# Performance work log

Hardware: AMD Instinct MI355X
Metric: run time of the kernel (lower is better)

The kernel has to match this reference:

```python
import jax, jax.numpy as jnp
import numpy as np

N_ATOMS = 200000
N_BONDS = 300000
E = 600000
D = 128
H = 128
EPS = 1e-5  # BatchNorm1d default eps


def setup_inputs() -> dict:
    key = jax.random.key(0)
    ks = jax.random.split(key, 8)
    x_atoms = jax.random.normal(ks[0], (N_ATOMS, D), jnp.float32)
    x_bonds = jax.random.normal(ks[1], (N_BONDS, D), jnp.float32)
    # atoms -> bonds edges: row0 src atom idx, row1 dst bond idx
    ei_ab = jnp.stack([
        jax.random.randint(ks[2], (E,), 0, N_ATOMS),
        jax.random.randint(ks[3], (E,), 0, N_BONDS),
    ]).astype(jnp.int64)
    # bonds -> atoms edges
    ei_ba = jnp.stack([
        jax.random.randint(ks[4], (E,), 0, N_BONDS),
        jax.random.randint(ks[5], (E,), 0, N_ATOMS),
    ]).astype(jnp.int64)
    xav = float(np.sqrt(6.0 / (D + H)))
    W = jax.random.uniform(ks[6], (H, D), jnp.float32, -xav, xav)   # shared lin_rel
    b = jnp.zeros((H,), jnp.float32)
    Wr = jax.random.uniform(ks[7], (H, D), jnp.float32, -xav, xav)  # res_connection
    br = jnp.zeros((H,), jnp.float32)
    return {
        "x_atoms": x_atoms, "x_bonds": x_bonds,
        "ei_ab": ei_ab, "ei_ba": ei_ba,
        "W": W, "b": b, "Wr": Wr, "br": br,
        "gamma_atoms": jnp.ones((H,), jnp.float32),
        "beta_atoms": jnp.zeros((H,), jnp.float32),
        "gamma_bonds": jnp.ones((H,), jnp.float32),
        "beta_bonds": jnp.zeros((H,), jnp.float32),
    }


def _bn(v, g, bt):
    # BatchNorm1d training-mode math: batch mean, biased variance
    m = v.mean(axis=0)
    var = v.var(axis=0)
    return (v - m) * jax.lax.rsqrt(var + EPS) * g + bt


def reference(x_atoms, x_bonds, ei_ab, ei_ba, W, b, Wr, br,
              gamma_atoms, beta_atoms, gamma_bonds, beta_bonds):
    # shared lin_rel applied to both node types
    h_atoms = x_atoms @ W.T + b   # [N_ATOMS, H]
    h_bonds = x_bonds @ W.T + b   # [N_BONDS, H]

    # message = lin(x_src)[src], aggregate = scatter-add at dst (source_to_target)
    agg_bonds = jax.ops.segment_sum(h_atoms[ei_ab[0]], ei_ab[1], num_segments=N_BONDS)
    agg_atoms = jax.ops.segment_sum(h_bonds[ei_ba[0]], ei_ba[1], num_segments=N_ATOMS)

    # residual: activation(res_connection(x))
    out_atoms = agg_atoms + jax.nn.relu(x_atoms @ Wr.T + br)
    out_bonds = agg_bonds + jax.nn.relu(x_bonds @ Wr.T + br)

    # dropout is identity in eval/deterministic reference
    out_atoms = _bn(out_atoms, gamma_atoms, beta_atoms)
    out_bonds = _bn(out_bonds, gamma_bonds, beta_bonds)
    return out_atoms, out_bonds
```

## Files before the change

kernel.cpp:

```cpp
#include <hip/hip_runtime.h>
#include <stdint.h>

#define NATOMS 200000
#define NBONDS 300000
#define NEDGE  600000
#define NSEG   (NATOMS + NBONDS)
#define DF     128
#define EPS    1e-5f
#define SCHUNK 2048
#define NSBLK  ((NSEG + SCHUNK - 1) / SCHUNK)
#define NBUCK  32
#define NCHA   (NATOMS / 64)
#define NCHB   ((NBONDS + 63) / 64)
#define NCH    (NCHA + NCHB)

typedef __attribute__((ext_vector_type(8))) short bf16x8;
typedef __attribute__((ext_vector_type(4))) float f32x4;
typedef unsigned short u16;

__device__ __forceinline__ short f2b(float f) {
  union { float f; uint32_t u; } v; v.f = f;
  uint32_t r = v.u + 0x7fffu + ((v.u >> 16) & 1u);
  return (short)(r >> 16);
}
__device__ __forceinline__ float bf2f(u16 h) {
  union { uint32_t u; float f; } v; v.u = ((uint32_t)h) << 16; return v.f;
}
__device__ __forceinline__ bf16x8 pack8(float4 u, float4 v) {
  bf16x8 t;
  t[0] = f2b(u.x); t[1] = f2b(u.y); t[2] = f2b(u.z); t[3] = f2b(u.w);
  t[4] = f2b(v.x); t[5] = f2b(v.y); t[6] = f2b(v.z); t[7] = f2b(v.w);
  return t;
}

__global__ void k_prep(const float* __restrict__ W, const float* __restrict__ Wr,
                       u16* __restrict__ Wb, u16* __restrict__ Wrb) {
  int i = blockIdx.x * blockDim.x + threadIdx.x;
  if (i < DF * DF) {
    Wb[i]  = (u16)f2b(W[i]);
    Wrb[i] = (u16)f2b(Wr[i]);
  }
}

__global__ void k_setup(const float* __restrict__ xa, const float* __restrict__ xb,
                        u16* __restrict__ xaT, u16* __restrict__ xbT,
                        const int* __restrict__ ab, const int* __restrict__ ba,
                        int* __restrict__ cnt,
                        const float* __restrict__ W, const float* __restrict__ Wr,
                        u16* __restrict__ Wb, u16* __restrict__ Wrb) {
  const int NA8 = NATOMS * DF / 8;
  const int NT8 = NSEG * DF / 8;
  int bid = blockIdx.x;
  if (bid < 4096) {
    int stride = 4096 * 256;
    for (int i = bid * 256 + threadIdx.x; i < NT8; i += stride) {
      const float* src; u16* dst; int j;
      if (i < NA8) { src = xa; dst = xaT; j = i; }
      else { src = xb; dst = xbT; j = i - NA8; }
      const float4 a = *(const float4*)(src + (size_t)j * 8);
      const float4 b = *(const float4*)(src + (size_t)j * 8 + 4);
      *(bf16x8*)(dst + (size_t)j * 8) = pack8(a, b);
    }
  } else if (bid < 4608) {
    int stride = 512 * 256;
    for (int e = (bid - 4096) * 256 + threadIdx.x; e < 2 * NEDGE; e += stride) {
      int g;
      if (e < NEDGE) g = NATOMS + ab[NEDGE + e];
      else           g = ba[NEDGE + (e - NEDGE)];
      atomicAdd(cnt + g, 1);
    }
  } else {
    int i = (bid - 4608) * 256 + threadIdx.x;
    if (i < DF * DF) {
      Wb[i]  = (u16)f2b(W[i]);
      Wrb[i] = (u16)f2b(Wr[i]);
    }
  }
}

__global__ void k_hist(const int* __restrict__ ab, const int* __restrict__ ba,
                       int* __restrict__ cnt) {
  int stride = gridDim.x * blockDim.x;
  for (int e = blockIdx.x * blockDim.x + threadIdx.x; e < 2 * NEDGE; e += stride) {
    int g;
    if (e < NEDGE) g = NATOMS + ab[NEDGE + e];
    else           g = ba[NEDGE + (e - NEDGE)];
    atomicAdd(cnt + g, 1);
  }
}

__global__ void k_scanA(const int* __restrict__ cnt, int* __restrict__ bsum) {
  __shared__ int wsm[4];
  int t = threadIdx.x;
  int base = blockIdx.x * SCHUNK + t * 8;
  int s = 0;
#pragma unroll
  for (int j = 0; j < 8; ++j) { int i = base + j; if (i < NSEG) s += cnt[i]; }
  for (int d = 1; d < 64; d <<= 1) s += __shfl_xor(s, d);
  if ((t & 63) == 0) wsm[t >> 6] = s;
  __syncthreads();
  if (t == 0) bsum[blockIdx.x] = wsm[0] + wsm[1] + wsm[2] + wsm[3];
}

__global__ void k_scanB(const int* __restrict__ bsum, int* __restrict__ bbase) {
  __shared__ int wsm[4];
  int t = threadIdx.x;
  int lane = t & 63;
  int v = (t < NSBLK) ? bsum[t] : 0;
  int s = v;
  for (int d = 1; d < 64; d <<= 1) { int n = __shfl_up(s, d); if (lane >= d) s += n; }
  if (lane == 63) wsm[t >> 6] = s;
  __syncthreads();
  int wbase = 0;
  for (int w = 0; w < (t >> 6); ++w) wbase += wsm[w];
  if (t < NSBLK) bbase[t] = wbase + s - v;
}

__global__ void k_scanC(const int* __restrict__ cnt, const int* __restrict__ bbase,
                        int* __restrict__ off, int* __restrict__ cursor) {
  __shared__ int wsm[4];
  int t = threadIdx.x;
  int lane = t & 63, wv = t >> 6;
  int base = blockIdx.x * SCHUNK + t * 8;
  int v[8]; int ts = 0;
#pragma unroll
  for (int j = 0; j < 8; ++j) { int i = base + j; v[j] = (i < NSEG) ? cnt[i] : 0; ts += v[j]; }
  int s = ts;
  for (int d = 1; d < 64; d <<= 1) { int n = __shfl_up(s, d); if (lane >= d) s += n; }
  if (lane == 63) wsm[wv] = s;
  __syncthreads();
  int wbase = bbase[blockIdx.x];
  for (int w = 0; w < wv; ++w) wbase += wsm[w];
  int run = wbase + s - ts;
#pragma unroll
  for (int j = 0; j < 8; ++j) {
    int i = base + j;
    if (i < NSEG) { off[i] = run; cursor[i] = run; }
    run += v[j];
  }
}

__global__ void k_fill(const int* __restrict__ ab, const int* __restrict__ ba,
                       int* __restrict__ cursor, int* __restrict__ sorted) {
  int stride = gridDim.x * blockDim.x;
  for (int e = blockIdx.x * blockDim.x + threadIdx.x; e < 2 * NEDGE; e += stride) {
    int g, src;
    if (e < NEDGE) { g = NATOMS + ab[NEDGE + e]; src = ab[e]; }
    else { int e2 = e - NEDGE; g = ba[NEDGE + e2]; src = ba[e2]; }
    int pos = atomicAdd(cursor + g, 1);
    sorted[pos] = src;
  }
}

__global__ __launch_bounds__(256) void k_fuse(
    const u16* __restrict__ xaT, const u16* __restrict__ xbT,
    const int* __restrict__ sorted, const int* __restrict__ off,
    const int* __restrict__ cnt, u16* __restrict__ gT,
    const u16* __restrict__ Wb, const u16* __restrict__ Wrb,
    const float* __restrict__ bb, const float* __restrict__ brb,
    float* __restrict__ stats) {
  __shared__ u16 aggL[64 * DF];

  int tid = threadIdx.x;
  int lane = tid & 63;
  int wv = tid >> 6;
  int r16 = lane & 15, kq = lane >> 4;
  int t016 = wv * 32;
  int qw = tid >> 4;
  int l16 = tid & 15;

  bf16x8 wf[2][4], wrf[2][4];
#pragma unroll
  for (int ti = 0; ti < 2; ++ti) {
#pragma unroll
    for (int kk = 0; kk < 4; ++kk) {
      size_t o = (size_t)(t016 + ti * 16 + r16) * DF + kk * 32 + kq * 8;
      wf[ti][kk]  = *(const bf16x8*)(Wb + o);
      wrf[ti][kk] = *(const bf16x8*)(Wrb + o);
    }
  }
  float bvv0 = bb[t016 + r16],      brr0 = brb[t016 + r16];
  float bvv1 = bb[t016 + 16 + r16], brr1 = brb[t016 + 16 + r16];

  float sA0 = 0.f, sA1 = 0.f, qA0 = 0.f, qA1 = 0.f;
  float sB0 = 0.f, sB1 = 0.f, qB0 = 0.f, qB1 = 0.f;

  for (int c = blockIdx.x; c < NCH; c += gridDim.x) {
    int typ, nrows, goff, base;
    if (c < NCHA) { typ = 0; nrows = NATOMS; goff = 0; base = c * 64; }
    else { typ = 1; nrows = NBONDS; goff = NATOMS; base = (c - NCHA) * 64; }
    const u16* gsrc = typ ? xaT : xbT;
    const u16* xsrc = typ ? xbT : xaT;

    __syncthreads();

#pragma unroll
    for (int i = 0; i < 4; ++i) {
      int r = qw + i * 16;
      int row = base + r;
      if (row < nrows) {
        int gidx = goff + row;
        int start = off[gidx], deg = cnt[gidx];
        float a0 = 0.f, a1 = 0.f, a2 = 0.f, a3 = 0.f;
        float a4 = 0.f, a5 = 0.f, a6 = 0.f, a7 = 0.f;
        int k = 0;
        for (; k + 1 < deg; k += 2) {
          int s0 = sorted[start + k], s1 = sorted[start + k + 1];
          bf16x8 v0 = *(const bf16x8*)(gsrc + (size_t)s0 * DF + l16 * 8);
          bf16x8 v1 = *(const bf16x8*)(gsrc + (size_t)s1 * DF + l16 * 8);
          a0 += bf2f((u16)v0[0]) + bf2f((u16)v1[0]);
          a1 += bf2f((u16)v0[1]) + bf2f((u16)v1[1]);
          a2 += bf2f((u16)v0[2]) + bf2f((u16)v1[2]);
          a3 += bf2f((u16)v0[3]) + bf2f((u16)v1[3]);
          a4 += bf2f((u16)v0[4]) + bf2f((u16)v1[4]);
          a5 += bf2f((u16)v0[5]) + bf2f((u16)v1[5]);
          a6 += bf2f((u16)v0[6]) + bf2f((u16)v1[6]);
          a7 += bf2f((u16)v0[7]) + bf2f((u16)v1[7]);
        }
        if (k < deg) {
          int s0 = sorted[start + k];
          bf16x8 v0 = *(const bf16x8*)(gsrc + (size_t)s0 * DF + l16 * 8);
          a0 += bf2f((u16)v0[0]); a1 += bf2f((u16)v0[1]);
          a2 += bf2f((u16)v0[2]); a3 += bf2f((u16)v0[3]);
          a4 += bf2f((u16)v0[4]); a5 += bf2f((u16)v0[5]);
          a6 += bf2f((u16)v0[6]); a7 += bf2f((u16)v0[7]);
        }
        bf16x8 rr;
        rr[0] = f2b(a0); rr[1] = f2b(a1); rr[2] = f2b(a2); rr[3] = f2b(a3);
        rr[4] = f2b(a4); rr[5] = f2b(a5); rr[6] = f2b(a6); rr[7] = f2b(a7);
        *(bf16x8*)(aggL + r * DF + ((l16 ^ (r & 7)) * 8)) = rr;
      }
    }
    __syncthreads();

#pragma unroll
    for (int rg = 0; rg < 4; ++rg) {
      int rowbase = base + rg * 16;
      if (rowbase < nrows) {
        int lrow = rg * 16 + r16;
        bf16x8 fA[4], fX[4];
#pragma unroll
        for (int kk = 0; kk < 4; ++kk) {
          int c8 = (4 * kk + kq) ^ (r16 & 7);
          fA[kk] = *(const bf16x8*)(aggL + lrow * DF + c8 * 8);
        }
        const u16* xp = xsrc + (size_t)(rowbase + r16) * DF + kq * 8;
#pragma unroll
        for (int kk = 0; kk < 4; ++kk) fX[kk] = *(const bf16x8*)(xp + kk * 32);

        f32x4 w0 = {0.f,0.f,0.f,0.f}, w1 = {0.f,0.f,0.f,0.f};
        f32x4 r0 = {0.f,0.f,0.f,0.f}, r1 = {0.f,0.f,0.f,0.f};
#pragma unroll
        for (int kk = 0; kk < 4; ++kk) {
          w0 = __builtin_amdgcn_mfma_f32_16x16x32_bf16(fA[kk], wf[0][kk], w0, 0, 0, 0);
          w1 = __builtin_amdgcn_mfma_f32_16x16x32_bf16(fA[kk], wf[1][kk], w1, 0, 0, 0);
          r0 = __builtin_amdgcn_mfma_f32_16x16x32_bf16(fX[kk], wrf[0][kk], r0, 0, 0, 0);
          r1 = __builtin_amdgcn_mfma_f32_16x16x32_bf16(fX[kk], wrf[1][kk], r1, 0, 0, 0);
        }

        float cf0 = (float)cnt[goff + rowbase + kq * 4 + 0];
        float cf1 = (float)cnt[goff + rowbase + kq * 4 + 1];
        float cf2 = (float)cnt[goff + rowbase + kq * 4 + 2];
        float cf3 = (float)cnt[goff + rowbase + kq * 4 + 3];

        u16* gp = gT + ((size_t)(goff + rowbase + kq * 4) << 7) + t016 + r16;
        float g0, g1, g2, g3, ss, qq;
        g0 = w0[0] + cf0 * bvv0 + fmaxf(r0[0] + brr0, 0.f);
        g1 = w0[1] + cf1 * bvv0 + fmaxf(r0[1] + brr0, 0.f);
        g2 = w0[2] + cf2 * bvv0 + fmaxf(r0[2] + brr0, 0.f);
        g3 = w0[3] + cf3 * bvv0 + fmaxf(r0[3] + brr0, 0.f);
        gp[0]   = (u16)f2b(g0); gp[128] = (u16)f2b(g1);
        gp[256] = (u16)f2b(g2); gp[384] = (u16)f2b(g3);
        ss = g0 + g1 + g2 + g3;
        qq = g0*g0 + g1*g1 + g2*g2 + g3*g3;
        if (typ) { sB0 += ss; qB0 += qq; } else { sA0 += ss; qA0 += qq; }
        g0 = w1[0] + cf0 * bvv1 + fmaxf(r1[0] + brr1, 0.f);
        g1 = w1[1] + cf1 * bvv1 + fmaxf(r1[1] + brr1, 0.f);
        g2 = w1[2] + cf2 * bvv1 + fmaxf(r1[2] + brr1, 0.f);
        g3 = w1[3] + cf3 * bvv1 + fmaxf(r1[3] + brr1, 0.f);
        gp[16]  = (u16)f2b(g0); gp[144] = (u16)f2b(g1);
        gp[272] = (u16)f2b(g2); gp[400] = (u16)f2b(g3);
        ss = g0 + g1 + g2 + g3;
        qq = g0*g0 + g1*g1 + g2*g2 + g3*g3;
        if (typ) { sB1 += ss; qB1 += qq; } else { sA1 += ss; qA1 += qq; }
      }
    }
  }

  int bkt = blockIdx.x & (NBUCK - 1);
  float* p = stats + (size_t)bkt * 4 * DF;
  {
    float s0 = sA0, q0 = qA0, s1 = sB0, q1 = qB0;
    s0 += __shfl_xor(s0, 16); q0 += __shfl_xor(q0, 16);
    s1 += __shfl_xor(s1, 16); q1 += __shfl_xor(q1, 16);
    s0 += __shfl_xor(s0, 32); q0 += __shfl_xor(q0, 32);
    s1 += __shfl_xor(s1, 32); q1 += __shfl_xor(q1, 32);
    if (kq == 0) {
      int feat = t016 + r16;
      atomicAdd(p + 0 * DF + feat, s0);
      atomicAdd(p + 1 * DF + feat, q0);
      atomicAdd(p + 2 * DF + feat, s1);
      atomicAdd(p + 3 * DF + feat, q1);
    }
  }
  {
    float s0 = sA1, q0 = qA1, s1 = sB1, q1 = qB1;
    s0 += __shfl_xor(s0, 16); q0 += __shfl_xor(q0, 16);
    s1 += __shfl_xor(s1, 16); q1 += __shfl_xor(q1, 16);
    s0 += __shfl_xor(s0, 32); q0 += __shfl_xor(q0, 32);
    s1 += __shfl_xor(s1, 32); q1 += __shfl_xor(q1, 32);
    if (kq == 0) {
      int feat = t016 + 16 + r16;
      atomicAdd(p + 0 * DF + feat, s0);
      atomicAdd(p + 1 * DF + feat, q0);
      atomicAdd(p + 2 * DF + feat, s1);
      atomicAdd(p + 3 * DF + feat, q1);
    }
  }
}

__global__ void k_gather_f(const float* __restrict__ xa, const float* __restrict__ xb,
                           const int* __restrict__ sorted, const int* __restrict__ off,
                           const int* __restrict__ cnt, float* __restrict__ outf) {
  int l32 = threadIdx.x & 31;
  int hwid = (blockIdx.x * blockDim.x + threadIdx.x) >> 5;
  int nhw = (gridDim.x * blockDim.x) >> 5;
  for (int g = hwid; g < NSEG; g += nhw) {
    int start = off[g], deg = cnt[g];
    const float* src = (g < NATOMS) ? xb : xa;
    float a0 = 0.f, a1 = 0.f, a2 = 0.f, a3 = 0.f;
    int k = 0;
    for (; k + 1 < deg; k += 2) {
      int s0 = sorted[start + k], s1 = sorted[start + k + 1];
      float4 v0 = *(const float4*)(src + (size_t)s0 * DF + l32 * 4);
      float4 v1 = *(const float4*)(src + (size_t)s1 * DF + l32 * 4);
      a0 += v0.x + v1.x; a1 += v0.y + v1.y; a2 += v0.z + v1.z; a3 += v0.w + v1.w;
    }
    if (k < deg) {
      int s0 = sorted[start + k];
      float4 v0 = *(const float4*)(src + (size_t)s0 * DF + l32 * 4);
      a0 += v0.x; a1 += v0.y; a2 += v0.z; a3 += v0.w;
    }
    float4 r; r.x = a0; r.y = a1; r.z = a2; r.w = a3;
    *(float4*)(outf + (size_t)g * DF + l32 * 4) = r;
  }
}

__global__ __launch_bounds__(256) void k_gemm0(
    const float* __restrict__ xa, const float* __restrict__ xb,
    float* __restrict__ outf, const int* __restrict__ cnt,
    const u16* __restrict__ Wb, const u16* __restrict__ Wrb,
    const float* __restrict__ bb, const float* __restrict__ brb,
    float* __restrict__ stats) {
  int lane = threadIdx.x & 63;
  int wv = threadIdx.x >> 6;
  int r16 = lane & 15, kq = lane >> 4;
  int t016 = wv * 32;

  bf16x8 wf[2][4], wrf[2][4];
#pragma unroll
  for (int ti = 0; ti < 2; ++ti) {
#pragma unroll
    for (int kk = 0; kk < 4; ++kk) {
      size_t o = (size_t)(t016 + ti * 16 + r16) * DF + kk * 32 + kq * 8;
      wf[ti][kk]  = *(const bf16x8*)(Wb + o);
      wrf[ti][kk] = *(const bf16x8*)(Wrb + o);
    }
  }
  float bvv[2] = { bb[t016 + r16], bb[t016 + 16 + r16] };
  float brr[2] = { brb[t016 + r16], brb[t016 + 16 + r16] };

  float sA[2] = {0.f, 0.f}, qA[2] = {0.f, 0.f};
  float sB[2] = {0.f, 0.f}, qB[2] = {0.f, 0.f};

  for (int c = blockIdx.x; c < NCH; c += gridDim.x) {
    int typ, nrows, goff, base;
    if (c < NCHA) { typ = 0; nrows = NATOMS; goff = 0; base = c * 64; }
    else { typ = 1; nrows = NBONDS; goff = NATOMS; base = (c - NCHA) * 64; }
    const float* xsrc = typ ? xb : xa;

#pragma unroll
    for (int rg = 0; rg < 4; ++rg) {
      int rowbase = base + rg * 16;
      if (rowbase < nrows) {
        int row = rowbase + r16;
        const float* ap = outf + (size_t)(goff + row) * DF + kq * 8;
        const float* xp = xsrc + (size_t)row * DF + kq * 8;
        bf16x8 fA[4], fX[4];
#pragma unroll
        for (int kk = 0; kk < 4; ++kk) {
          fA[kk] = pack8(*(const float4*)(ap + kk * 32), *(const float4*)(ap + kk * 32 + 4));
          fX[kk] = pack8(*(const float4*)(xp + kk * 32), *(const float4*)(xp + kk * 32 + 4));
        }
        __syncthreads();

        f32x4 accW[2], accR[2];
#pragma unroll
        for (int ti = 0; ti < 2; ++ti) {
#pragma unroll
          for (int r = 0; r < 4; ++r) { accW[ti][r] = 0.f; accR[ti][r] = 0.f; }
        }
#pragma unroll
        for (int kk = 0; kk < 4; ++kk) {
#pragma unroll
          for (int ti = 0; ti < 2; ++ti) {
            accW[ti] = __builtin_amdgcn_mfma_f32_16x16x32_bf16(fA[kk], wf[ti][kk], accW[ti], 0, 0, 0);
            accR[ti] = __builtin_amdgcn_mfma_f32_16x16x32_bf16(fX[kk], wrf[ti][kk], accR[ti], 0, 0, 0);
          }
        }
        float cf[4];
#pragma unroll
        for (int r = 0; r < 4; ++r)
          cf[r] = (float)cnt[goff + rowbase + kq * 4 + r];
#pragma unroll
        for (int ti = 0; ti < 2; ++ti) {
          int feat = t016 + ti * 16 + r16;
          float s = 0.f, q = 0.f;
#pragma unroll
          for (int r = 0; r < 4; ++r) {
            int grow = rowbase + kq * 4 + r;
            float gg = accW[ti][r] + cf[r] * bvv[ti] + fmaxf(accR[ti][r] + brr[ti], 0.f);
            outf[(size_t)(goff + grow) * DF + feat] = gg;
            s += gg; q += gg * gg;
          }
          if (typ == 0) { sA[ti] += s; qA[ti] += q; }
          else          { sB[ti] += s; qB[ti] += q; }
        }
      }
    }
  }

  int bkt = blockIdx.x & (NBUCK - 1);
  float* p = stats + (size_t)bkt * 4 * DF;
#pragma unroll
  for (int ti = 0; ti < 2; ++ti) {
    float s0 = sA[ti], q0 = qA[ti], s1 = sB[ti], q1 = qB[ti];
    s0 += __shfl_xor(s0, 16); q0 += __shfl_xor(q0, 16);
    s1 += __shfl_xor(s1, 16); q1 += __shfl_xor(q1, 16);
    s0 += __shfl_xor(s0, 32); q0 += __shfl_xor(q0, 32);
    s1 += __shfl_xor(s1, 32); q1 += __shfl_xor(q1, 32);
    if (kq == 0) {
      int feat = t016 + ti * 16 + r16;
      atomicAdd(p + 0 * DF + feat, s0);
      atomicAdd(p + 1 * DF + feat, q0);
      atomicAdd(p + 2 * DF + feat, s1);
      atomicAdd(p + 3 * DF + feat, q1);
    }
  }
}

__global__ void k_stats(const float* __restrict__ stats,
                        const float* __restrict__ ga, const float* __restrict__ bea,
                        const float* __restrict__ gb, const float* __restrict__ beb,
                        float* __restrict__ scale, float* __restrict__ shift) {
  int tid = threadIdx.x;
  if (tid < 2 * DF) {
    int t = tid >> 7, f = tid & (DF - 1);
    float S = 0.f, SS = 0.f;
    for (int bk = 0; bk < NBUCK; ++bk) {
      const float* p = stats + (size_t)bk * 4 * DF;
      S  += p[(2 * t) * DF + f];
      SS += p[(2 * t + 1) * DF + f];
    }
    float n = t ? (float)NBONDS : (float)NATOMS;
    float mean = S / n;
    float var = SS / n - mean * mean;
    float rstd = rsqrtf(var + EPS);
    float g = t ? gb[f] : ga[f];
    float be = t ? beb[f] : bea[f];
    scale[tid] = rstd * g;
    shift[tid] = be - mean * rstd * g;
  }
}

template<int TIER>
__global__ void k_norm(float* __restrict__ out, const u16* __restrict__ gT,
                       const float* __restrict__ scale, const float* __restrict__ shift) {
  if constexpr (TIER) {
    const size_t nv = (size_t)NSEG * DF / 8;
    size_t stride = (size_t)gridDim.x * blockDim.x;
    for (size_t i = (size_t)blockIdx.x * blockDim.x + threadIdx.x; i < nv; i += stride) {
      size_t e = i * 8;
      int t = e >= (size_t)NATOMS * DF;
      int f = (int)(e & (DF - 1));
      bf16x8 v = *(const bf16x8*)(gT + e);
      const float* sc = scale + t * DF + f;
      const float* sh = shift + t * DF + f;
      float4 o0, o1;
      o0.x = fmaf(bf2f((u16)v[0]), sc[0], sh[0]);
      o0.y = fmaf(bf2f((u16)v[1]), sc[1], sh[1]);
      o0.z = fmaf(bf2f((u16)v[2]), sc[2], sh[2]);
      o0.w = fmaf(bf2f((u16)v[3]), sc[3], sh[3]);
      o1.x = fmaf(bf2f((u16)v[4]), sc[4], sh[4]);
      o1.y = fmaf(bf2f((u16)v[5]), sc[5], sh[5]);
      o1.z = fmaf(bf2f((u16)v[6]), sc[6], sh[6]);
      o1.w = fmaf(bf2f((u16)v[7]), sc[7], sh[7]);
      *(float4*)(out + e) = o0;
      *(float4*)(out + e + 4) = o1;
    }
  } else {
    const size_t nv = (size_t)NSEG * DF / 4;
    size_t stride = (size_t)gridDim.x * blockDim.x;
    for (size_t i = (size_t)blockIdx.x * blockDim.x + threadIdx.x; i < nv; i += stride) {
      size_t e = i * 4;
      int t = e >= (size_t)NATOMS * DF;
      int f = (int)(e & (DF - 1));
      const float* sc = scale + t * DF + f;
      const float* sh = shift + t * DF + f;
      float4 v = ((float4*)out)[i];
      v.x = fmaf(v.x, sc[0], sh[0]);
      v.y = fmaf(v.y, sc[1], sh[1]);
      v.z = fmaf(v.z, sc[2], sh[2]);
      v.w = fmaf(v.w, sc[3], sh[3]);
      ((float4*)out)[i] = v;
    }
  }
}

extern "C" void kernel_launch(void* const* d_in, const int* in_sizes, int n_in,
                              void* d_out, int out_size, void* d_ws, size_t ws_size,
                              hipStream_t stream) {
  const float* xa  = (const float*)d_in[0];
  const float* xb  = (const float*)d_in[1];
  const int*   ab  = (const int*)d_in[2];
  const int*   ba  = (const int*)d_in[3];
  const float* W   = (const float*)d_in[4];
  const float* b   = (const float*)d_in[5];
  const float* Wr  = (const float*)d_in[6];
  const float* br  = (const float*)d_in[7];
  const float* ga  = (const float*)d_in[8];
  const float* bea = (const float*)d_in[9];
  const float* gb  = (const float*)d_in[10];
  const float* beb = (const float*)d_in[11];
  float* out = (float*)d_out;

  char* ws = (char*)d_ws;
  int*   cnt    = (int*)ws;
  int*   off    = (int*)(ws +  2000000);
  int*   cursor = (int*)(ws +  4000000);
  int*   sorted = (int*)(ws +  6000000);
  float* stats  = (float*)(ws + 10800000);
  int*   bsum   = (int*)(ws + 10865536);
  int*   bbase  = (int*)(ws + 10866560);
  u16*   Wbf    = (u16*)(ws + 10867584);
  u16*   Wrbf   = (u16*)(ws + 10900352);
  float* scale  = (float*)(ws + 10933120);
  float* shift  = (float*)(ws + 10934144);
  u16*   gT   = (u16*)(ws + 10935168);
  u16*   xaT  = (u16*)(ws + 138935168);
  u16*   xbT  = (u16*)(ws + 190135168);
  const bool xt = ws_size >= 266935168ull;

  hipMemsetAsync(cnt, 0, 2000000, stream);
  hipMemsetAsync(stats, 0, 65536, stream);

  if (xt) {
    k_setup<<<4672, 256, 0, stream>>>(xa, xb, xaT, xbT, ab, ba, cnt, W, Wr, Wbf, Wrbf);
  } else {
    k_prep<<<64, 256, 0, stream>>>(W, Wr, Wbf, Wrbf);
    k_hist<<<2048, 256, 0, stream>>>(ab, ba, cnt);
  }
  k_scanA<<<NSBLK, 256, 0, stream>>>(cnt, bsum);
  k_scanB<<<1, 256, 0, stream>>>(bsum, bbase);
  k_scanC<<<NSBLK, 256, 0, stream>>>(cnt, bbase, off, cursor);
  k_fill<<<2048, 256, 0, stream>>>(ab, ba, cursor, sorted);

  if (xt) {
    k_fuse<<<2048, 256, 0, stream>>>(xaT, xbT, sorted, off, cnt, gT,
                                     Wbf, Wrbf, b, br, stats);
    k_stats<<<1, 256, 0, stream>>>(stats, ga, bea, gb, beb, scale, shift);
    k_norm<1><<<4096, 256, 0, stream>>>(out, gT, scale, shift);
  } else {
    k_gather_f<<<8192, 256, 0, stream>>>(xa, xb, sorted, off, cnt, out);
    k_gemm0<<<2048, 256, 0, stream>>>(xa, xb, out, cnt, Wbf, Wrbf, b, br, stats);
    k_stats<<<1, 256, 0, stream>>>(stats, ga, bea, gb, beb, scale, shift);
    k_norm<0><<<8192, 256, 0, stream>>>(out, gT, scale, shift);
  }
}
```

Before: 552.6 us.

## Double-buffer aggregation tile and overlap gather with previous chunk's MFMA

Gives the fused kernel two LDS aggregation buffers so the gather of chunk c runs before the MFMA/epilogue of chunk c-1, with one barrier per iteration instead of two. The gather loop is also restructured so each thread walks its four rows together, issuing up to four independent row loads per step to expose more memory-level parallelism. The cost is doubled LDS use (32 KB), more registers for the four accumulators, and predicated work bounded by the largest degree among the four rows.

```diff
diff --git a/kernel.cpp b/kernel.cpp
--- a/kernel.cpp
+++ b/kernel.cpp
@@ -152,6 +152,68 @@
   }
 }
 
+#define PHASE_B(TY, NR, GO, BA, XS, BUF) {                                          \
+  _Pragma("unroll")                                                                 \
+  for (int rg = 0; rg < 4; ++rg) {                                                  \
+    int rowbase = (BA) + rg * 16;                                                   \
+    if (rowbase < (NR)) {                                                           \
+      int lrow = rg * 16 + r16;                                                     \
+      int sx = r16 & 7;                                                             \
+      bf16x8 fA0 = *(const bf16x8*)((BUF) + lrow * DF + (((0  + kq) ^ sx) * 8));    \
+      bf16x8 fA1 = *(const bf16x8*)((BUF) + lrow * DF + (((4  + kq) ^ sx) * 8));    \
+      bf16x8 fA2 = *(const bf16x8*)((BUF) + lrow * DF + (((8  + kq) ^ sx) * 8));    \
+      bf16x8 fA3 = *(const bf16x8*)((BUF) + lrow * DF + (((12 + kq) ^ sx) * 8));    \
+      const u16* xp_ = (XS) + (size_t)(rowbase + r16) * DF + kq * 8;                \
+      bf16x8 fX0 = *(const bf16x8*)(xp_);                                           \
+      bf16x8 fX1 = *(const bf16x8*)(xp_ + 32);                                      \
+      bf16x8 fX2 = *(const bf16x8*)(xp_ + 64);                                      \
+      bf16x8 fX3 = *(const bf16x8*)(xp_ + 96);                                      \
+      f32x4 bw0 = {0.f,0.f,0.f,0.f}, bw1 = {0.f,0.f,0.f,0.f};                       \
+      f32x4 bre0 = {0.f,0.f,0.f,0.f}, bre1 = {0.f,0.f,0.f,0.f};                     \
+      bw0 = __builtin_amdgcn_mfma_f32_16x16x32_bf16(fA0, wf[0][0], bw0, 0,0,0);     \
+      bw1 = __builtin_amdgcn_mfma_f32_16x16x32_bf16(fA0, wf[1][0], bw1, 0,0,0);     \
+      bre0 = __builtin_amdgcn_mfma_f32_16x16x32_bf16(fX0, wrf[0][0], bre0, 0,0,0);  \
+      bre1 = __builtin_amdgcn_mfma_f32_16x16x32_bf16(fX0, wrf[1][0], bre1, 0,0,0);  \
+      bw0 = __builtin_amdgcn_mfma_f32_16x16x32_bf16(fA1, wf[0][1], bw0, 0,0,0);     \
+      bw1 = __builtin_amdgcn_mfma_f32_16x16x32_bf16(fA1, wf[1][1], bw1, 0,0,0);     \
+      bre0 = __builtin_amdgcn_mfma_f32_16x16x32_bf16(fX1, wrf[0][1], bre0, 0,0,0);  \
+      bre1 = __builtin_amdgcn_mfma_f32_16x16x32_bf16(fX1, wrf[1][1], bre1, 0,0,0);  \
+      bw0 = __builtin_amdgcn_mfma_f32_16x16x32_bf16(fA2, wf[0][2], bw0, 0,0,0);     \
+      bw1 = __builtin_amdgcn_mfma_f32_16x16x32_bf16(fA2, wf[1][2], bw1, 0,0,0);     \
+      bre0 = __builtin_amdgcn_mfma_f32_16x16x32_bf16(fX2, wrf[0][2], bre0, 0,0,0);  \
+      bre1 = __builtin_amdgcn_mfma_f32_16x16x32_bf16(fX2, wrf[1][2], bre1, 0,0,0);  \
+      bw0 = __builtin_amdgcn_mfma_f32_16x16x32_bf16(fA3, wf[0][3], bw0, 0,0,0);     \
+      bw1 = __builtin_amdgcn_mfma_f32_16x16x32_bf16(fA3, wf[1][3], bw1, 0,0,0);     \
+      bre0 = __builtin_amdgcn_mfma_f32_16x16x32_bf16(fX3, wrf[0][3], bre0, 0,0,0);  \
+      bre1 = __builtin_amdgcn_mfma_f32_16x16x32_bf16(fX3, wrf[1][3], bre1, 0,0,0);  \
+      float cf0 = (float)cnt[(GO) + rowbase + kq * 4 + 0];                          \
+      float cf1 = (float)cnt[(GO) + rowbase + kq * 4 + 1];                          \
+      float cf2 = (float)cnt[(GO) + rowbase + kq * 4 + 2];                          \
+      float cf3 = (float)cnt[(GO) + rowbase + kq * 4 + 3];                          \
+      u16* gp = gT + ((size_t)((GO) + rowbase + kq * 4) << 7) + t016 + r16;         \
+      float g0, g1, g2, g3, ss, qq;                                                 \
+      g0 = bw0[0] + cf0 * bvv0 + fmaxf(bre0[0] + brr0, 0.f);                        \
+      g1 = bw0[1] + cf1 * bvv0 + fmaxf(bre0[1] + brr0, 0.f);                        \
+      g2 = bw0[2] + cf2 * bvv0 + fmaxf(bre0[2] + brr0, 0.f);                        \
+      g3 = bw0[3] + cf3 * bvv0 + fmaxf(bre0[3] + brr0, 0.f);                        \
+      gp[0]   = (u16)f2b(g0); gp[128] = (u16)f2b(g1);                               \
+      gp[256] = (u16)f2b(g2); gp[384] = (u16)f2b(g3);                               \
+      ss = g0 + g1 + g2 + g3;                                                       \
+      qq = g0*g0 + g1*g1 + g2*g2 + g3*g3;                                           \
+      if (TY) { sB0 += ss; qB0 += qq; } else { sA0 += ss; qA0 += qq; }              \
+      g0 = bw1[0] + cf0 * bvv1 + fmaxf(bre1[0] + brr1, 0.f);                        \
+      g1 = bw1[1] + cf1 * bvv1 + fmaxf(bre1[1] + brr1, 0.f);                        \
+      g2 = bw1[2] + cf2 * bvv1 + fmaxf(bre1[2] + brr1, 0.f);                        \
+      g3 = bw1[3] + cf3 * bvv1 + fmaxf(bre1[3] + brr1, 0.f);                        \
+      gp[16]  = (u16)f2b(g0); gp[144] = (u16)f2b(g1);                               \
+      gp[272] = (u16)f2b(g2); gp[400] = (u16)f2b(g3);                               \
+      ss = g0 + g1 + g2 + g3;                                                       \
+      qq = g0*g0 + g1*g1 + g2*g2 + g3*g3;                                           \
+      if (TY) { sB1 += ss; qB1 += qq; } else { sA1 += ss; qA1 += qq; }              \
+    }                                                                               \
+  }                                                                                 \
+}
+
 __global__ __launch_bounds__(256) void k_fuse(
     const u16* __restrict__ xaT, const u16* __restrict__ xbT,
     const int* __restrict__ sorted, const int* __restrict__ off,
@@ -159,7 +221,7 @@
     const u16* __restrict__ Wb, const u16* __restrict__ Wrb,
     const float* __restrict__ bb, const float* __restrict__ brb,
     float* __restrict__ stats) {
-  __shared__ u16 aggL[64 * DF];
+  __shared__ u16 aggL[2][64 * DF];
 
   int tid = threadIdx.x;
   int lane = tid & 63;
@@ -185,6 +247,11 @@
   float sA0 = 0.f, sA1 = 0.f, qA0 = 0.f, qA1 = 0.f;
   float sB0 = 0.f, sB1 = 0.f, qB0 = 0.f, qB1 = 0.f;
 
+  int pb = 0;
+  int pTyp = 0, pNrows = 0, pGoff = 0, pBase = 0;
+  const u16* pXsrc = xaT;
+  bool hasPrev = false;
+
   for (int c = blockIdx.x; c < NCH; c += gridDim.x) {
     int typ, nrows, goff, base;
     if (c < NCHA) { typ = 0; nrows = NATOMS; goff = 0; base = c * 64; }
@@ -192,99 +259,83 @@
     const u16* gsrc = typ ? xaT : xbT;
     const u16* xsrc = typ ? xbT : xaT;
 
+    {
+      int vr0 = base + qw, vr1 = vr0 + 16, vr2 = vr0 + 32, vr3 = vr0 + 48;
+      int s0 = 0, s1 = 0, s2 = 0, s3 = 0, d0 = 0, d1 = 0, d2 = 0, d3 = 0;
+      if (vr0 < nrows) { s0 = off[goff + vr0]; d0 = cnt[goff + vr0]; }
+      if (vr1 < nrows) { s1 = off[goff + vr1]; d1 = cnt[goff + vr1]; }
+      if (vr2 < nrows) { s2 = off[goff + vr2]; d2 = cnt[goff + vr2]; }
+      if (vr3 < nrows) { s3 = off[goff + vr3]; d3 = cnt[goff + vr3]; }
+      float A0[8], A1[8], A2[8], A3[8];
+#pragma unroll
+      for (int j = 0; j < 8; ++j) { A0[j] = 0.f; A1[j] = 0.f; A2[j] = 0.f; A3[j] = 0.f; }
+      int dmax = max(max(d0, d1), max(d2, d3));
+      const u16* gp16 = gsrc + l16 * 8;
+      for (int k = 0; k < dmax; ++k) {
+        int i0 = (k < d0) ? sorted[s0 + k] : -1;
+        int i1 = (k < d1) ? sorted[s1 + k] : -1;
+        int i2 = (k < d2) ? sorted[s2 + k] : -1;
+        int i3 = (k < d3) ? sorted[s3 + k] : -1;
+        bf16x8 v0, v1, v2, v3;
+        if (i0 >= 0) v0 = *(const bf16x8*)(gp16 + (size_t)i0 * DF);
+        if (i1 >= 0) v1 = *(const bf16x8*)(gp16 + (size_t)i1 * DF);
+        if (i2 >= 0) v2 = *(const bf16x8*)(gp16 + (size_t)i2 * DF);
+        if (i3 >= 0) v3 = *(const bf16x8*)(gp16 + (size_t)i3 * DF);
+        if (i0 >= 0) {
+#pragma unroll
+          for (int j = 0; j < 8; ++j) A0[j] += bf2f((u16)v0[j]);
+        }
+        if (i1 >= 0) {
+#pragma unroll
+          for (int j = 0; j < 8; ++j) A1[j] += bf2f((u16)v1[j]);
+        }
+        if (i2 >= 0) {
+#pragma unroll
+          for (int j = 0; j < 8; ++j) A2[j] += bf2f((u16)v2[j]);
+        }
+        if (i3 >= 0) {
+#pragma unroll
+          for (int j = 0; j < 8; ++j) A3[j] += bf2f((u16)v3[j]);
+        }
+      }
+      int swz = (l16 ^ (qw & 7)) * 8;
+      u16* bufp = aggL[pb];
+      if (vr0 < nrows) {
+        bf16x8 rr;
+#pragma unroll
+        for (int j = 0; j < 8; ++j) rr[j] = f2b(A0[j]);
+        *(bf16x8*)(bufp + (qw +  0) * DF + swz) = rr;
+      }
+      if (vr1 < nrows) {
+        bf16x8 rr;
+#pragma unroll
+        for (int j = 0; j < 8; ++j) rr[j] = f2b(A1[j]);
+        *(bf16x8*)(bufp + (qw + 16) * DF + swz) = rr;
+      }
+      if (vr2 < nrows) {
+        bf16x8 rr;
+#pragma unroll
+        for (int j = 0; j < 8; ++j) rr[j] = f2b(A2[j]);
+        *(bf16x8*)(bufp + (qw + 32) * DF + swz) = rr;
+      }
+      if (vr3 < nrows) {
+        bf16x8 rr;
+#pragma unroll
+        for (int j = 0; j < 8; ++j) rr[j] = f2b(A3[j]);
+        *(bf16x8*)(bufp + (qw + 48) * DF + swz) = rr;
+      }
+    }
+
+    if (hasPrev) {
+      PHASE_B(pTyp, pNrows, pGoff, pBase, pXsrc, aggL[pb ^ 1])
+    }
     __syncthreads();
 
-#pragma unroll
-    for (int i = 0; i < 4; ++i) {
-      int r = qw + i * 16;
-      int row = base + r;
-      if (row < nrows) {
-        int gidx = goff + row;
-        int start = off[gidx], deg = cnt[gidx];
-        float a0 = 0.f, a1 = 0.f, a2 = 0.f, a3 = 0.f;
-        float a4 = 0.f, a5 = 0.f, a6 = 0.f, a7 = 0.f;
-        int k = 0;
-        for (; k + 1 < deg; k += 2) {
-          int s0 = sorted[start + k], s1 = sorted[start + k + 1];
-          bf16x8 v0 = *(const bf16x8*)(gsrc + (size_t)s0 * DF + l16 * 8);
-          bf16x8 v1 = *(const bf16x8*)(gsrc + (size_t)s1 * DF + l16 * 8);
-          a0 += bf2f((u16)v0[0]) + bf2f((u16)v1[0]);
-          a1 += bf2f((u16)v0[1]) + bf2f((u16)v1[1]);
-          a2 += bf2f((u16)v0[2]) + bf2f((u16)v1[2]);
-          a3 += bf2f((u16)v0[3]) + bf2f((u16)v1[3]);
-          a4 += bf2f((u16)v0[4]) + bf2f((u16)v1[4]);
-          a5 += bf2f((u16)v0[5]) + bf2f((u16)v1[5]);
-          a6 += bf2f((u16)v0[6]) + bf2f((u16)v1[6]);
-          a7 += bf2f((u16)v0[7]) + bf2f((u16)v1[7]);
-        }
-        if (k < deg) {
-          int s0 = sorted[start + k];
-          bf16x8 v0 = *(const bf16x8*)(gsrc + (size_t)s0 * DF + l16 * 8);
-          a0 += bf2f((u16)v0[0]); a1 += bf2f((u16)v0[1]);
-          a2 += bf2f((u16)v0[2]); a3 += bf2f((u16)v0[3]);
-          a4 += bf2f((u16)v0[4]); a5 += bf2f((u16)v0[5]);
-          a6 += bf2f((u16)v0[6]); a7 += bf2f((u16)v0[7]);
-        }
-        bf16x8 rr;
-        rr[0] = f2b(a0); rr[1] = f2b(a1); rr[2] = f2b(a2); rr[3] = f2b(a3);
-        rr[4] = f2b(a4); rr[5] = f2b(a5); rr[6] = f2b(a6); rr[7] = f2b(a7);
-        *(bf16x8*)(aggL + r * DF + ((l16 ^ (r & 7)) * 8)) = rr;
-      }
-    }
-    __syncthreads();
-
-#pragma unroll
-    for (int rg = 0; rg < 4; ++rg) {
-      int rowbase = base + rg * 16;
-      if (rowbase < nrows) {
-        int lrow = rg * 16 + r16;
-        bf16x8 fA[4], fX[4];
-#pragma unroll
-        for (int kk = 0; kk < 4; ++kk) {
-          int c8 = (4 * kk + kq) ^ (r16 & 7);
-          fA[kk] = *(const bf16x8*)(aggL + lrow * DF + c8 * 8);
-        }
-        const u16* xp = xsrc + (size_t)(rowbase + r16) * DF + kq * 8;
-#pragma unroll
-        for (int kk = 0; kk < 4; ++kk) fX[kk] = *(const bf16x8*)(xp + kk * 32);
-
-        f32x4 w0 = {0.f,0.f,0.f,0.f}, w1 = {0.f,0.f,0.f,0.f};
-        f32x4 r0 = {0.f,0.f,0.f,0.f}, r1 = {0.f,0.f,0.f,0.f};
-#pragma unroll
-        for (int kk = 0; kk < 4; ++kk) {
-          w0 = __builtin_amdgcn_mfma_f32_16x16x32_bf16(fA[kk], wf[0][kk], w0, 0, 0, 0);
-          w1 = __builtin_amdgcn_mfma_f32_16x16x32_bf16(fA[kk], wf[1][kk], w1, 0, 0, 0);
-          r0 = __builtin_amdgcn_mfma_f32_16x16x32_bf16(fX[kk], wrf[0][kk], r0, 0, 0, 0);
-          r1 = __builtin_amdgcn_mfma_f32_16x16x32_bf16(fX[kk], wrf[1][kk], r1, 0, 0, 0);
-        }
-
-        float cf0 = (float)cnt[goff + rowbase + kq * 4 + 0];
-        float cf1 = (float)cnt[goff + rowbase + kq * 4 + 1];
-        float cf2 = (float)cnt[goff + rowbase + kq * 4 + 2];
-        float cf3 = (float)cnt[goff + rowbase + kq * 4 + 3];
-
-        u16* gp = gT + ((size_t)(goff + rowbase + kq * 4) << 7) + t016 + r16;
-        float g0, g1, g2, g3, ss, qq;
-        g0 = w0[0] + cf0 * bvv0 + fmaxf(r0[0] + brr0, 0.f);
-        g1 = w0[1] + cf1 * bvv0 + fmaxf(r0[1] + brr0, 0.f);
-        g2 = w0[2] + cf2 * bvv0 + fmaxf(r0[2] + brr0, 0.f);
-        g3 = w0[3] + cf3 * bvv0 + fmaxf(r0[3] + brr0, 0.f);
-        gp[0]   = (u16)f2b(g0); gp[128] = (u16)f2b(g1);
-        gp[256] = (u16)f2b(g2); gp[384] = (u16)f2b(g3);
-        ss = g0 + g1 + g2 + g3;
-        qq = g0*g0 + g1*g1 + g2*g2 + g3*g3;
-        if (typ) { sB0 += ss; qB0 += qq; } else { sA0 += ss; qA0 += qq; }
-        g0 = w1[0] + cf0 * bvv1 + fmaxf(r1[0] + brr1, 0.f);
-        g1 = w1[1] + cf1 * bvv1 + fmaxf(r1[1] + brr1, 0.f);
-        g2 = w1[2] + cf2 * bvv1 + fmaxf(r1[2] + brr1, 0.f);
-        g3 = w1[3] + cf3 * bvv1 + fmaxf(r1[3] + brr1, 0.f);
-        gp[16]  = (u16)f2b(g0); gp[144] = (u16)f2b(g1);
-        gp[272] = (u16)f2b(g2); gp[400] = (u16)f2b(g3);
-        ss = g0 + g1 + g2 + g3;
-        qq = g0*g0 + g1*g1 + g2*g2 + g3*g3;
-        if (typ) { sB1 += ss; qB1 += qq; } else { sA1 += ss; qA1 += qq; }
-      }
-    }
+    pTyp = typ; pNrows = nrows; pGoff = goff; pBase = base; pXsrc = xsrc;
+    hasPrev = true; pb ^= 1;
+  }
+  if (hasPrev) {
+    PHASE_B(pTyp, pNrows, pGoff, pBase, pXsrc, aggL[pb ^ 1])
   }
 
   int bkt = blockIdx.x & (NBUCK - 1);
```

Measured after the change: 542.8 us. No clear change (-1.8%).
